# Kernel optimization log

Hardware: AMD Instinct MI355X
Metric: run time of the kernel (lower is better)

The kernel has to match this reference:

```python
import jax, jax.numpy as jnp
import numpy as np

N_SINKHORN_ITERS = 20
SINKHORN_EPS = 1e-08  # also used as eps for the dynamic-H RMS norm (per docstring)
RMSNORM_EPS = 1e-05
ALPHA_INIT = 0.01
B, N_STREAMS, C = 4096, 4, 4096


def sinkhorn_knopp(M, num_iters=N_SINKHORN_ITERS, eps=SINKHORN_EPS):
    # Iterative row/column normalization toward a doubly-stochastic matrix.
    def body(i, M):
        M = M / (jnp.sum(M, axis=-1, keepdims=True) + eps)
        M = M / (jnp.sum(M, axis=-2, keepdims=True) + eps)
        return M
    return jax.lax.fori_loop(0, num_iters, body, M)


def setup_inputs() -> dict:
    key = jax.random.key(0)
    ks = jax.random.split(key, 4)
    n, nC = N_STREAMS, N_STREAMS * C
    return {
        "x": jax.random.normal(ks[0], (B, n, C), dtype=jnp.float32),
        "rmsnorm_weight": jnp.ones((C,), dtype=jnp.float32),
        "phi_pre": jax.random.normal(ks[1], (n, nC), dtype=jnp.float32) * 0.02,
        "phi_post": jax.random.normal(ks[2], (n, nC), dtype=jnp.float32) * 0.02,
        "phi_res": jax.random.normal(ks[3], (n * n, nC), dtype=jnp.float32) * 0.02,
        "b_pre": jnp.zeros((n,), dtype=jnp.float32),
        "b_post": jnp.zeros((n,), dtype=jnp.float32),
        "b_res": jnp.zeros((n, n), dtype=jnp.float32),
        "alpha_pre": jnp.float32(ALPHA_INIT),
        "alpha_post": jnp.float32(ALPHA_INIT),
        "alpha_res": jnp.float32(ALPHA_INIT),
    }


def reference(x, rmsnorm_weight, phi_pre, phi_post, phi_res,
              b_pre, b_post, b_res, alpha_pre, alpha_post, alpha_res):
    Bd, n, Cd = x.shape
    # --- dynamic H projections from RMS-normalized flattened streams ---
    xf = x.reshape(Bd, n * Cd)                                   # [B, nC]
    xn = xf * jax.lax.rsqrt(jnp.mean(xf * xf, axis=-1, keepdims=True) + SINKHORN_EPS)
    h_pre = alpha_pre * (xn @ phi_pre.T) + b_pre                 # [B, n]
    h_post = alpha_post * (xn @ phi_post.T) + b_post             # [B, n]
    h_res = (alpha_res * (xn @ phi_res.T)).reshape(Bd, n, n) + b_res  # [B, n, n]
    # --- manifold constraints ---
    H_pre = jax.nn.softmax(h_pre, axis=-1)                       # simplex (aggregation weights)
    H_post = 2.0 * jax.nn.sigmoid(h_post)                        # gain in (0, 2), ~1 at init
    M = sinkhorn_knopp(jnp.exp(h_res))                           # doubly-stochastic mixing [B, n, n]
    # --- aggregate -> rmsnorm -> distribute + mix + add ---
    x_agg = jnp.einsum('bn,bnc->bc', H_pre, x)                   # [B, C]
    y_norm = x_agg * jax.lax.rsqrt(jnp.mean(x_agg * x_agg, axis=-1, keepdims=True) + RMSNORM_EPS)
    y_norm = y_norm * rmsnorm_weight
    out = H_post[..., None] * y_norm[:, None, :] + jnp.einsum('bij,bjc->bic', M, x)
    return out
```

## Files before the change

kernel.cpp:

```cpp
#include <hip/hip_runtime.h>
#include <math.h>

#define B_ROWS 4096
#define NSTR 4
#define C_DIM 4096
#define NC 16384
#define NC4 4096
#define C4 1024

#define ASYNC_COPY16(g, l)                                                     \
    __builtin_amdgcn_global_load_lds(                                         \
        (const __attribute__((address_space(1))) void*)(g),                   \
        (__attribute__((address_space(3))) void*)(l), 16, 0, 0)

__global__ void repack_kernel(
    const float4* __restrict__ pre4,
    const float4* __restrict__ post4,
    const float4* __restrict__ res4,
    float4* __restrict__ phiws4)
{
    const int idx = blockIdx.x * blockDim.x + threadIdx.x;
    if (idx >= 24 * NC4) return;
    const int row = idx / NC4;
    const int k4  = idx % NC4;
    float4 v;
    if (row < 4)        v = pre4[row * NC4 + k4];
    else if (row < 8)   v = post4[(row - 4) * NC4 + k4];
    else                v = res4[(row - 8) * NC4 + k4];
    phiws4[idx] = v;
}

__global__ __launch_bounds__(256, 4) void proj_kernel(
    const float* __restrict__ x,
    const float* __restrict__ phiws,
    float* __restrict__ dots_part)
{
    const float4* __restrict__ x4   = reinterpret_cast<const float4*>(x);
    const float4* __restrict__ phi4 = reinterpret_cast<const float4*>(phiws);

    const int bid  = blockIdx.x;
    const int kb   = bid & 1;
    const int b0   = (bid >> 1) * 4;
    const int wave = threadIdx.x >> 6;
    const int lane = threadIdx.x & 63;
    const int half = lane >> 5;
    const int l31  = lane & 31;
    const int wv   = __builtin_amdgcn_readfirstlane(wave);

    __shared__ float4 xs[2][4][256];
    __shared__ float  red[4][2][12];
    __shared__ float  redss[4];

    const int kbase = kb * 2048;

    const float4* __restrict__ srcw    = x4 + (size_t)(b0 + wave) * NC4 + kbase + lane;
    const float4* __restrict__ phibase = phi4 + (size_t)(wave * 6 + half * 3) * NC4 + kbase + l31;

    float acc[4][3];
#pragma unroll
    for (int r = 0; r < 4; ++r)
#pragma unroll
        for (int j = 0; j < 3; ++j) acc[r][j] = 0.f;
    float ssq = 0.f;

#pragma unroll
    for (int i = 0; i < 4; ++i)
        ASYNC_COPY16(srcw + i * 64, &xs[0][wave][i * 64]);
    __syncthreads();

    int cur = 0;
#pragma unroll 1
    for (int c = 0; c < 8; ++c) {
        if (c < 7) {
#pragma unroll
            for (int i = 0; i < 4; ++i)
                ASYNC_COPY16(srcw + (c + 1) * 256 + i * 64,
                             &xs[cur ^ 1][wave][i * 64]);
        }

        const float4* __restrict__ xl = &xs[cur][0][0];
        const float4* __restrict__ pb = phibase + c * 256;
#pragma unroll 2
        for (int u = 0; u < 8; ++u) {
            const float4 xv0 = xl[0 * 256 + u * 32 + l31];
            const float4 xv1 = xl[1 * 256 + u * 32 + l31];
            const float4 xv2 = xl[2 * 256 + u * 32 + l31];
            const float4 xv3 = xl[3 * 256 + u * 32 + l31];
            const float4 p0  = pb[(size_t)0 * NC4 + u * 32];
            const float4 p1  = pb[(size_t)1 * NC4 + u * 32];
            const float4 p2  = pb[(size_t)2 * NC4 + u * 32];

            acc[0][0] += xv0.x*p0.x + xv0.y*p0.y + xv0.z*p0.z + xv0.w*p0.w;
            acc[1][0] += xv1.x*p0.x + xv1.y*p0.y + xv1.z*p0.z + xv1.w*p0.w;
            acc[2][0] += xv2.x*p0.x + xv2.y*p0.y + xv2.z*p0.z + xv2.w*p0.w;
            acc[3][0] += xv3.x*p0.x + xv3.y*p0.y + xv3.z*p0.z + xv3.w*p0.w;

            acc[0][1] += xv0.x*p1.x + xv0.y*p1.y + xv0.z*p1.z + xv0.w*p1.w;
            acc[1][1] += xv1.x*p1.x + xv1.y*p1.y + xv1.z*p1.z + xv1.w*p1.w;
            acc[2][1] += xv2.x*p1.x + xv2.y*p1.y + xv2.z*p1.z + xv2.w*p1.w;
            acc[3][1] += xv3.x*p1.x + xv3.y*p1.y + xv3.z*p1.z + xv3.w*p1.w;

            acc[0][2] += xv0.x*p2.x + xv0.y*p2.y + xv0.z*p2.z + xv0.w*p2.w;
            acc[1][2] += xv1.x*p2.x + xv1.y*p2.y + xv1.z*p2.z + xv1.w*p2.w;
            acc[2][2] += xv2.x*p2.x + xv2.y*p2.y + xv2.z*p2.z + xv2.w*p2.w;
            acc[3][2] += xv3.x*p2.x + xv3.y*p2.y + xv3.z*p2.z + xv3.w*p2.w;

            float4 xw;
            if      (wv == 0) xw = xv0;
            else if (wv == 1) xw = xv1;
            else if (wv == 2) xw = xv2;
            else              xw = xv3;
            ssq += xw.x*xw.x + xw.y*xw.y + xw.z*xw.z + xw.w*xw.w;
        }

        __syncthreads();
        cur ^= 1;
    }

#pragma unroll
    for (int r = 0; r < 4; ++r)
#pragma unroll
        for (int j = 0; j < 3; ++j) {
            float v = acc[r][j];
#pragma unroll
            for (int off = 16; off > 0; off >>= 1)
                v += __shfl_xor(v, off, 64);
            acc[r][j] = v;
        }
#pragma unroll
    for (int off = 16; off > 0; off >>= 1)
        ssq += __shfl_xor(ssq, off, 64);

    if (l31 == 0) {
#pragma unroll
        for (int r = 0; r < 4; ++r)
#pragma unroll
            for (int j = 0; j < 3; ++j)
                red[wave][half][r * 3 + j] = acc[r][j];
    }
    if (lane == 0) redss[wave] = ssq;
    __syncthreads();

    const int t = threadIdx.x;
    if (t < 100) {
        const int r = t / 25, o = t % 25;
        float s;
        if (o < 24) {
            const int w  = o / 6;
            const int hf = (o % 6) / 3;
            const int j  = o % 3;
            s = red[w][hf][r * 3 + j];
        } else {
            s = redss[r];
        }
        dots_part[((size_t)kb * B_ROWS + (b0 + r)) * 25 + o] = s;
    }
}

__global__ void finalize_kernel(
    const float* __restrict__ dots_part,
    const float* __restrict__ b_pre,
    const float* __restrict__ b_post,
    const float* __restrict__ b_res,
    const float* __restrict__ alpha_pre,
    const float* __restrict__ alpha_post,
    const float* __restrict__ alpha_res,
    float* __restrict__ params)
{
    const int row = blockIdx.x * blockDim.x + threadIdx.x;
    if (row >= B_ROWS) return;

    const float* d0 = dots_part + (size_t)row * 25;
    const float* d1 = dots_part + ((size_t)B_ROWS + row) * 25;
    float d[25];
#pragma unroll
    for (int o = 0; o < 25; ++o) d[o] = d0[o] + d1[o];

    const float inv_rms = rsqrtf(d[24] * (1.f / (float)NC) + 1e-8f);
    const float ap  = alpha_pre[0];
    const float apo = alpha_post[0];
    const float ar  = alpha_res[0];

    float hp[4];
    float mx = -1e30f;
#pragma unroll
    for (int j = 0; j < 4; ++j) {
        hp[j] = ap * d[j] * inv_rms + b_pre[j];
        mx = fmaxf(mx, hp[j]);
    }
    float e[4], s = 0.f;
#pragma unroll
    for (int j = 0; j < 4; ++j) { e[j] = expf(hp[j] - mx); s += e[j]; }
    float Hpre[4];
#pragma unroll
    for (int j = 0; j < 4; ++j) Hpre[j] = e[j] / s;

    float Hpost[4];
#pragma unroll
    for (int j = 0; j < 4; ++j) {
        const float h = apo * d[4 + j] * inv_rms + b_post[j];
        Hpost[j] = 2.f / (1.f + expf(-h));
    }

    float M[16];
#pragma unroll
    for (int k = 0; k < 16; ++k)
        M[k] = expf(ar * d[8 + k] * inv_rms + b_res[k]);

    for (int it = 0; it < 20; ++it) {
#pragma unroll
        for (int i = 0; i < 4; ++i) {
            const float rs = M[i*4+0] + M[i*4+1] + M[i*4+2] + M[i*4+3] + 1e-8f;
#pragma unroll
            for (int j = 0; j < 4; ++j) M[i*4+j] = M[i*4+j] / rs;
        }
#pragma unroll
        for (int j = 0; j < 4; ++j) {
            const float cs = M[0*4+j] + M[1*4+j] + M[2*4+j] + M[3*4+j] + 1e-8f;
#pragma unroll
            for (int i = 0; i < 4; ++i) M[i*4+j] = M[i*4+j] / cs;
        }
    }

    float* p = params + (size_t)row * 24;
#pragma unroll
    for (int j = 0; j < 4; ++j)  p[j]     = Hpre[j];
#pragma unroll
    for (int j = 0; j < 4; ++j)  p[4 + j] = Hpost[j];
#pragma unroll
    for (int k = 0; k < 16; ++k) p[8 + k] = M[k];
}

__global__ __launch_bounds__(256, 2) void out_kernel(
    const float* __restrict__ x,
    const float* __restrict__ w,
    const float* __restrict__ params,
    float* __restrict__ out)
{
    const float4* __restrict__ x4 = reinterpret_cast<const float4*>(x);
    const float4* __restrict__ w4 = reinterpret_cast<const float4*>(w);
    float4* __restrict__ out4 = reinterpret_cast<float4*>(out);

    const int b = blockIdx.x;
    const float* __restrict__ p = params + (size_t)b * 24;

    float Hpre[4], Hpost[4], M[16];
#pragma unroll
    for (int j = 0; j < 4; ++j)  Hpre[j]  = p[j];
#pragma unroll
    for (int j = 0; j < 4; ++j)  Hpost[j] = p[4 + j];
#pragma unroll
    for (int k = 0; k < 16; ++k) M[k]     = p[8 + k];

    const int t = threadIdx.x;
    const size_t base = (size_t)b * NC4;

    float4 xv[4][4];
    float4 agg[4];
    float ssq = 0.f;

#pragma unroll
    for (int u = 0; u < 4; ++u) {
        const int c4 = u * 256 + t;
#pragma unroll
        for (int n = 0; n < 4; ++n)
            xv[u][n] = x4[base + (size_t)n * C4 + c4];

        float4 a;
        a.x = Hpre[0]*xv[u][0].x + Hpre[1]*xv[u][1].x + Hpre[2]*xv[u][2].x + Hpre[3]*xv[u][3].x;
        a.y = Hpre[0]*xv[u][0].y + Hpre[1]*xv[u][1].y + Hpre[2]*xv[u][2].y + Hpre[3]*xv[u][3].y;
        a.z = Hpre[0]*xv[u][0].z + Hpre[1]*xv[u][1].z + Hpre[2]*xv[u][2].z + Hpre[3]*xv[u][3].z;
        a.w = Hpre[0]*xv[u][0].w + Hpre[1]*xv[u][1].w + Hpre[2]*xv[u][2].w + Hpre[3]*xv[u][3].w;
        agg[u] = a;
        ssq += a.x*a.x + a.y*a.y + a.z*a.z + a.w*a.w;
    }

#pragma unroll
    for (int off = 32; off > 0; off >>= 1)
        ssq += __shfl_xor(ssq, off, 64);
    __shared__ float red[4];
    if ((t & 63) == 0) red[t >> 6] = ssq;
    __syncthreads();
    const float total = red[0] + red[1] + red[2] + red[3];
    const float inv = rsqrtf(total * (1.f / (float)C_DIM) + 1e-5f);

#pragma unroll
    for (int u = 0; u < 4; ++u) {
        const int c4 = u * 256 + t;
        const float4 wv = w4[c4];
        float4 y;
        y.x = agg[u].x * inv * wv.x;
        y.y = agg[u].y * inv * wv.y;
        y.z = agg[u].z * inv * wv.z;
        y.w = agg[u].w * inv * wv.w;

#pragma unroll
        for (int i = 0; i < 4; ++i) {
            float4 o;
            o.x = Hpost[i]*y.x + M[i*4+0]*xv[u][0].x + M[i*4+1]*xv[u][1].x
                               + M[i*4+2]*xv[u][2].x + M[i*4+3]*xv[u][3].x;
            o.y = Hpost[i]*y.y + M[i*4+0]*xv[u][0].y + M[i*4+1]*xv[u][1].y
                               + M[i*4+2]*xv[u][2].y + M[i*4+3]*xv[u][3].y;
            o.z = Hpost[i]*y.z + M[i*4+0]*xv[u][0].z + M[i*4+1]*xv[u][1].z
                               + M[i*4+2]*xv[u][2].z + M[i*4+3]*xv[u][3].z;
            o.w = Hpost[i]*y.w + M[i*4+0]*xv[u][0].w + M[i*4+1]*xv[u][1].w
                               + M[i*4+2]*xv[u][2].w + M[i*4+3]*xv[u][3].w;
            out4[base + (size_t)i * C4 + c4] = o;
        }
    }
}

extern "C" void kernel_launch(void* const* d_in, const int* in_sizes, int n_in,
                              void* d_out, int out_size, void* d_ws, size_t ws_size,
                              hipStream_t stream) {
    const float* x        = (const float*)d_in[0];
    const float* w        = (const float*)d_in[1];
    const float* phi_pre  = (const float*)d_in[2];
    const float* phi_post = (const float*)d_in[3];
    const float* phi_res  = (const float*)d_in[4];
    const float* b_pre    = (const float*)d_in[5];
    const float* b_post   = (const float*)d_in[6];
    const float* b_res    = (const float*)d_in[7];
    const float* a_pre    = (const float*)d_in[8];
    const float* a_post   = (const float*)d_in[9];
    const float* a_res    = (const float*)d_in[10];
    float* out = (float*)d_out;

    float* dots_part = (float*)d_ws;
    float* params    = dots_part + (size_t)2 * B_ROWS * 25;
    float* phiws     = params + (size_t)B_ROWS * 24;

    hipLaunchKernelGGL(repack_kernel, dim3((24 * NC4 + 255) / 256), dim3(256), 0, stream,
                       (const float4*)phi_pre, (const float4*)phi_post,
                       (const float4*)phi_res, (float4*)phiws);
    hipLaunchKernelGGL(proj_kernel, dim3(B_ROWS / 2), dim3(256), 0, stream,
                       x, phiws, dots_part);
    hipLaunchKernelGGL(finalize_kernel, dim3(B_ROWS / 256), dim3(256), 0, stream,
                       dots_part, b_pre, b_post, b_res, a_pre, a_post, a_res, params);
    hipLaunchKernelGGL(out_kernel, dim3(B_ROWS), dim3(256), 0, stream,
                       x, w, params, out);
}
```

Measured before the change: 233.5 us.

## Retile projection kernel to 8 rows per block with 512 threads

```diff
diff --git a/kernel.cpp b/kernel.cpp
--- a/kernel.cpp
+++ b/kernel.cpp
@@ -30,7 +30,7 @@
     phiws4[idx] = v;
 }
 
-__global__ __launch_bounds__(256, 4) void proj_kernel(
+__global__ __launch_bounds__(512, 4) void proj_kernel(
     const float* __restrict__ x,
     const float* __restrict__ phiws,
     float* __restrict__ dots_part)
@@ -40,25 +40,23 @@
 
     const int bid  = blockIdx.x;
     const int kb   = bid & 1;
-    const int b0   = (bid >> 1) * 4;
+    const int b0   = (bid >> 1) * 8;
     const int wave = threadIdx.x >> 6;
     const int lane = threadIdx.x & 63;
-    const int half = lane >> 5;
-    const int l31  = lane & 31;
     const int wv   = __builtin_amdgcn_readfirstlane(wave);
 
-    __shared__ float4 xs[2][4][256];
-    __shared__ float  red[4][2][12];
-    __shared__ float  redss[4];
+    __shared__ float4 xs[2][8][256];
+    __shared__ float  red[8][8][3];
+    __shared__ float  redss[8];
 
     const int kbase = kb * 2048;
 
     const float4* __restrict__ srcw    = x4 + (size_t)(b0 + wave) * NC4 + kbase + lane;
-    const float4* __restrict__ phibase = phi4 + (size_t)(wave * 6 + half * 3) * NC4 + kbase + l31;
-
-    float acc[4][3];
-#pragma unroll
-    for (int r = 0; r < 4; ++r)
+    const float4* __restrict__ phibase = phi4 + (size_t)(wave * 3) * NC4 + kbase + lane;
+
+    float acc[8][3];
+#pragma unroll
+    for (int r = 0; r < 8; ++r)
 #pragma unroll
         for (int j = 0; j < 3; ++j) acc[r][j] = 0.f;
     float ssq = 0.f;
@@ -78,39 +76,25 @@
                              &xs[cur ^ 1][wave][i * 64]);
         }
 
-        const float4* __restrict__ xl = &xs[cur][0][0];
         const float4* __restrict__ pb = phibase + c * 256;
-#pragma unroll 2
-        for (int u = 0; u < 8; ++u) {
-            const float4 xv0 = xl[0 * 256 + u * 32 + l31];
-            const float4 xv1 = xl[1 * 256 + u * 32 + l31];
-            const float4 xv2 = xl[2 * 256 + u * 32 + l31];
-            const float4 xv3 = xl[3 * 256 + u * 32 + l31];
-            const float4 p0  = pb[(size_t)0 * NC4 + u * 32];
-            const float4 p1  = pb[(size_t)1 * NC4 + u * 32];
-            const float4 p2  = pb[(size_t)2 * NC4 + u * 32];
-
-            acc[0][0] += xv0.x*p0.x + xv0.y*p0.y + xv0.z*p0.z + xv0.w*p0.w;
-            acc[1][0] += xv1.x*p0.x + xv1.y*p0.y + xv1.z*p0.z + xv1.w*p0.w;
-            acc[2][0] += xv2.x*p0.x + xv2.y*p0.y + xv2.z*p0.z + xv2.w*p0.w;
-            acc[3][0] += xv3.x*p0.x + xv3.y*p0.y + xv3.z*p0.z + xv3.w*p0.w;
-
-            acc[0][1] += xv0.x*p1.x + xv0.y*p1.y + xv0.z*p1.z + xv0.w*p1.w;
-            acc[1][1] += xv1.x*p1.x + xv1.y*p1.y + xv1.z*p1.z + xv1.w*p1.w;
-            acc[2][1] += xv2.x*p1.x + xv2.y*p1.y + xv2.z*p1.z + xv2.w*p1.w;
-            acc[3][1] += xv3.x*p1.x + xv3.y*p1.y + xv3.z*p1.z + xv3.w*p1.w;
-
-            acc[0][2] += xv0.x*p2.x + xv0.y*p2.y + xv0.z*p2.z + xv0.w*p2.w;
-            acc[1][2] += xv1.x*p2.x + xv1.y*p2.y + xv1.z*p2.z + xv1.w*p2.w;
-            acc[2][2] += xv2.x*p2.x + xv2.y*p2.y + xv2.z*p2.z + xv2.w*p2.w;
-            acc[3][2] += xv3.x*p2.x + xv3.y*p2.y + xv3.z*p2.z + xv3.w*p2.w;
-
-            float4 xw;
-            if      (wv == 0) xw = xv0;
-            else if (wv == 1) xw = xv1;
-            else if (wv == 2) xw = xv2;
-            else              xw = xv3;
+#pragma unroll 1
+        for (int u = 0; u < 4; ++u) {
+            const int ki = u * 64 + lane;
+
+            const float4 p0 = pb[(size_t)0 * NC4 + u * 64];
+            const float4 p1 = pb[(size_t)1 * NC4 + u * 64];
+            const float4 p2 = pb[(size_t)2 * NC4 + u * 64];
+
+            const float4 xw = xs[cur][wv][ki];
             ssq += xw.x*xw.x + xw.y*xw.y + xw.z*xw.z + xw.w*xw.w;
+
+#pragma unroll
+            for (int r = 0; r < 8; ++r) {
+                const float4 xv = xs[cur][r][ki];
+                acc[r][0] += xv.x*p0.x + xv.y*p0.y + xv.z*p0.z + xv.w*p0.w;
+                acc[r][1] += xv.x*p1.x + xv.y*p1.y + xv.z*p1.z + xv.w*p1.w;
+                acc[r][2] += xv.x*p2.x + xv.y*p2.y + xv.z*p2.z + xv.w*p2.w;
+            }
         }
 
         __syncthreads();
@@ -118,41 +102,35 @@
     }
 
 #pragma unroll
-    for (int r = 0; r < 4; ++r)
+    for (int r = 0; r < 8; ++r)
 #pragma unroll
         for (int j = 0; j < 3; ++j) {
             float v = acc[r][j];
 #pragma unroll
-            for (int off = 16; off > 0; off >>= 1)
+            for (int off = 32; off > 0; off >>= 1)
                 v += __shfl_xor(v, off, 64);
             acc[r][j] = v;
         }
 #pragma unroll
-    for (int off = 16; off > 0; off >>= 1)
+    for (int off = 32; off > 0; off >>= 1)
         ssq += __shfl_xor(ssq, off, 64);
 
-    if (l31 == 0) {
-#pragma unroll
-        for (int r = 0; r < 4; ++r)
+    if (lane == 0) {
+#pragma unroll
+        for (int r = 0; r < 8; ++r)
 #pragma unroll
             for (int j = 0; j < 3; ++j)
-                red[wave][half][r * 3 + j] = acc[r][j];
-    }
-    if (lane == 0) redss[wave] = ssq;
+                red[wave][r][j] = acc[r][j];
+        redss[wave] = ssq;
+    }
     __syncthreads();
 
     const int t = threadIdx.x;
-    if (t < 100) {
+    if (t < 200) {
         const int r = t / 25, o = t % 25;
         float s;
-        if (o < 24) {
-            const int w  = o / 6;
-            const int hf = (o % 6) / 3;
-            const int j  = o % 3;
-            s = red[w][hf][r * 3 + j];
-        } else {
-            s = redss[r];
-        }
+        if (o < 24) s = red[o / 3][r][o % 3];
+        else        s = redss[r];
         dots_part[((size_t)kb * B_ROWS + (b0 + r)) * 25 + o] = s;
     }
 }
@@ -333,7 +311,7 @@
     hipLaunchKernelGGL(repack_kernel, dim3((24 * NC4 + 255) / 256), dim3(256), 0, stream,
                        (const float4*)phi_pre, (const float4*)phi_post,
                        (const float4*)phi_res, (float4*)phiws);
-    hipLaunchKernelGGL(proj_kernel, dim3(B_ROWS / 2), dim3(256), 0, stream,
+    hipLaunchKernelGGL(proj_kernel, dim3(B_ROWS / 4), dim3(512), 0, stream,
                        x, phiws, dots_part);
     hipLaunchKernelGGL(finalize_kernel, dim3(B_ROWS / 256), dim3(256), 0, stream,
                        dots_part, b_pre, b_post, b_res, a_pre, a_post, a_res, params);
```

New measurement: 228.3 us. -2.2%, faster.
